# Optimization experiments

Hardware: AMD Instinct MI355X
Metric: run time of the kernel (lower is better)

## Reference

```python
import jax, jax.numpy as jnp
import numpy as np

WBITS_MAX = 3.0   # 3-bit signed narrow-range weights: levels in [-3, 3]
ABITS_MAX = 15.0  # 4-bit unsigned activations: levels in [0, 15]


def round_ste(x):
    # straight-through estimator for round (Brevitas uses STE)
    return x + jax.lax.stop_gradient(jnp.round(x) - x)


def quant_weight(w):
    # per-tensor symmetric narrow-range 3-bit fake quant (Int weight per-tensor float)
    s = jnp.max(jnp.abs(w)) / WBITS_MAX
    wq = jnp.clip(round_ste(w / s), -WBITS_MAX, WBITS_MAX) * s
    return wq, s


def quant_bias(b, w_scale, in_step):
    # Brevitas BiasQuant: bias scale = input_scale * weight_scale, no clipping (wide int)
    sb = w_scale * in_step  # in_step is shape (1,)
    return round_ste(b / sb) * sb


def quant_relu(x, s):
    # QuantReLU(bit_width=4): relu then unsigned 4-bit fake quant with learned scale s
    step = s / ABITS_MAX
    return jnp.clip(round_ste(jax.nn.relu(x) / step), 0.0, ABITS_MAX) * step


def conv2d(x, w):
    return jax.lax.conv_general_dilated(
        x, w, window_strides=(1, 1), padding='VALID',
        dimension_numbers=('NCHW', 'OIHW', 'NCHW'))


def maxpool2(x):
    return jax.lax.reduce_window(x, -jnp.inf, jax.lax.max,
                                 (1, 1, 2, 2), (1, 1, 2, 2), 'VALID')


def setup_inputs() -> dict:
    key = jax.random.key(0)
    ks = jax.random.split(key, 16)
    d = {}
    d['x'] = jax.random.normal(ks[0], (256, 3, 160, 160), jnp.float32)
    d['w1'] = jax.random.normal(ks[1], (6, 3, 3, 3), jnp.float32) * 0.2
    d['w2'] = jax.random.normal(ks[2], (12, 6, 3, 3), jnp.float32) * 0.2
    d['b2'] = jax.random.normal(ks[3], (12,), jnp.float32) * 0.1
    d['w3'] = jax.random.normal(ks[4], (18, 12, 3, 3), jnp.float32) * 0.2
    d['b3'] = jax.random.normal(ks[5], (18,), jnp.float32) * 0.1
    d['w4'] = jax.random.normal(ks[6], (18, 18, 3, 3), jnp.float32) * 0.2
    d['b4'] = jax.random.normal(ks[7], (18,), jnp.float32) * 0.1
    d['w5'] = jax.random.normal(ks[8], (18, 18, 3, 3), jnp.float32) * 0.2
    d['b5'] = jax.random.normal(ks[9], (18,), jnp.float32) * 0.1
    d['fw1'] = jax.random.normal(ks[10], (120, 162), jnp.float32) * 0.1
    d['fb1'] = jax.random.normal(ks[11], (120,), jnp.float32) * 0.1
    d['fw2'] = jax.random.normal(ks[12], (84, 120), jnp.float32) * 0.1
    d['fb2'] = jax.random.normal(ks[13], (84,), jnp.float32) * 0.1
    d['fw3'] = jax.random.normal(ks[14], (9, 84), jnp.float32) * 0.1
    for i in range(1, 8):
        d[f's{i}'] = jnp.full((1,), 6.0, jnp.float32)  # learned act scales (calibrated init)
    return d


def reference(x, w1, w2, b2, w3, b3, w4, b4, w5, b5,
              fw1, fb1, fw2, fb2, fw3, s1, s2, s3, s4, s5, s6, s7):
    # stage 1 (note: original forward feeds raw x into conv1, bypassing quant_inp)
    q1, _ = quant_weight(w1)
    out = maxpool2(quant_relu(conv2d(x, q1), s1))            # [B,6,79,79]
    # stage 2
    q2, ws2 = quant_weight(w2)
    bq2 = quant_bias(b2, ws2, s1 / ABITS_MAX)
    out = maxpool2(quant_relu(conv2d(out, q2) + bq2[None, :, None, None], s2))  # [B,12,38,38]
    # stage 3
    q3, ws3 = quant_weight(w3)
    bq3 = quant_bias(b3, ws3, s2 / ABITS_MAX)
    out = maxpool2(quant_relu(conv2d(out, q3) + bq3[None, :, None, None], s3))  # [B,18,18,18]
    # stage 4
    q4, ws4 = quant_weight(w4)
    bq4 = quant_bias(b4, ws4, s3 / ABITS_MAX)
    out = maxpool2(quant_relu(conv2d(out, q4) + bq4[None, :, None, None], s4))  # [B,18,8,8]
    # stage 5
    q5, ws5 = quant_weight(w5)
    bq5 = quant_bias(b5, ws5, s4 / ABITS_MAX)
    out = maxpool2(quant_relu(conv2d(out, q5) + bq5[None, :, None, None], s5))  # [B,18,3,3]
    out = out.reshape(out.shape[0], -1)                      # [B,162]
    # fc1
    qf1, fs1 = quant_weight(fw1)
    bqf1 = quant_bias(fb1, fs1, s5 / ABITS_MAX)
    out = quant_relu(out @ qf1.T + bqf1, s6)                 # [B,120]
    # fc2
    qf2, fs2 = quant_weight(fw2)
    bqf2 = quant_bias(fb2, fs2, s6 / ABITS_MAX)
    out = quant_relu(out @ qf2.T + bqf2, s7)                 # [B,84]
    # fc3 (no bias, output not re-quantized: return_quant_tensor=False default path)
    qf3, _ = quant_weight(fw3)
    return out @ qf3.T                                       # [B,9]
```

## Files before the change

### kernel.cpp

```cpp
#include <hip/hip_runtime.h>
#include <hip/hip_bf16.h>
#include <math.h>
#include <type_traits>

constexpr size_t OFF_OUT1B = 0;
constexpr size_t OFF_OUT2B = (size_t)256 * 6 * 79 * 80;
constexpr size_t OFF_A3B   = 0;

template<int CIN, int COUT, int NCO, int HIN, int WSIN,
         int HPOOL, int WPOOL, int WSOUT, int XG, int RB,
         int THREADS, bool HAS_BIAS, bool IN_U8>
__global__ __launch_bounds__(THREADS)
void conv_stage(const void* __restrict__ in_,
                const float* __restrict__ w_raw,
                const float* __restrict__ b_raw,
                const float* __restrict__ s_prev,
                const float* __restrict__ s_act,
                unsigned char* __restrict__ out)
{
    using TIN = typename std::conditional<IN_U8, unsigned char, float>::type;
    constexpr int GROUPS = COUT / NCO;
    constexpr int W4IN   = WSIN / 4;
    constexpr int NW     = COUT * CIN * 9;
    constexpr int STEPS  = 4 * CIN;
    static_assert(NCO * GROUPS == COUT, "NCO divides COUT");
    static_assert(GROUPS * XG * RB <= THREADS, "single compute pass");
    static_assert(4 * XG == WSOUT, "full padded row coverage");
    static_assert(WSIN % 4 == 0, "vec4 loads");

    __shared__ float lw[NW];
    __shared__ float lb[COUT];
    __shared__ float red[THREADS];

    const int r0  = blockIdx.x * RB;
    const int n   = blockIdx.y;
    const int tid = threadIdx.x;

    float mx = 0.0f;
    for (int i = tid; i < NW; i += THREADS) {
        const float v = w_raw[i];
        lw[i] = v;
        mx = fmaxf(mx, fabsf(v));
    }
    if (HAS_BIAS)
        for (int i = tid; i < COUT; i += THREADS) lb[i] = b_raw[i];
    red[tid] = mx;
    __syncthreads();
    for (int s = THREADS / 2; s > 0; s >>= 1) {
        if (tid < s) red[tid] = fmaxf(red[tid], red[tid + s]);
        __syncthreads();
    }
    const float sw_ = red[0] / 3.0f;
    for (int i = tid; i < NW; i += THREADS) {
        float q = rintf(lw[i] / sw_);
        q = fminf(fmaxf(q, -3.0f), 3.0f);
        lw[i] = q * sw_;
    }
    if (HAS_BIAS) {
        const float sb = sw_ * (s_prev[0] / 15.0f);
        for (int i = tid; i < COUT; i += THREADS)
            lb[i] = rintf(lb[i] / sb) * sb;
    }
    __syncthreads();

    const int o = tid;
    if (o >= GROUPS * XG * RB) return;
    const int cog = o % GROUPS;
    const int xg  = (o / GROUPS) % XG;
    const int ry  = o / (GROUPS * XG);
    const int r   = r0 + ry;
    if (r >= HPOOL) return;

    const float step = s_act[0] / 15.0f;
    float step_in = 0.0f;
    if constexpr (IN_U8) step_in = s_prev[0] / 15.0f;

    const int u0 = 2 * xg;
    const int u1 = 2 * xg + 1;
    const int u2 = (2 * xg + 2 < W4IN) ? (2 * xg + 2) : (W4IN - 1);

    const TIN* in   = (const TIN*)in_;
    const TIN* base = in + (size_t)n * CIN * HIN * WSIN + (size_t)(2 * r) * WSIN;

    float acc[NCO][16];
#pragma unroll
    for (int j = 0; j < NCO; ++j)
#pragma unroll
        for (int i = 0; i < 16; ++i) acc[j][i] = 0.0f;

    float4       fbuf[3][3];
    unsigned int ubuf[3][3];
    float        wv[NCO][9];

#define ISSUE_STEP(S)                                                          \
    {                                                                          \
        const TIN* rp = base + (size_t)((S) >> 2) * HIN * WSIN                 \
                             + (size_t)((S) & 3) * WSIN;                       \
        if constexpr (IN_U8) {                                                 \
            ubuf[(S) % 3][0] = *(const unsigned int*)&rp[4 * u0];              \
            ubuf[(S) % 3][1] = *(const unsigned int*)&rp[4 * u1];              \
            ubuf[(S) % 3][2] = *(const unsigned int*)&rp[4 * u2];              \
        } else {                                                               \
            fbuf[(S) % 3][0] = *(const float4*)&rp[4 * u0];                    \
            fbuf[(S) % 3][1] = *(const float4*)&rp[4 * u1];                    \
            fbuf[(S) % 3][2] = *(const float4*)&rp[4 * u2];                    \
        }                                                                      \
    }

    ISSUE_STEP(0);
    ISSUE_STEP(1);

#pragma unroll
    for (int s = 0; s < STEPS; ++s) {
        const int c  = s >> 2;
        const int rr = s & 3;

        if (s + 2 < STEPS) ISSUE_STEP(s + 2);

        if (rr == 0) {
#pragma unroll
            for (int j = 0; j < NCO; ++j)
#pragma unroll
                for (int k = 0; k < 9; ++k)
                    wv[j][k] = lw[((NCO * cog + j) * CIN + c) * 9 + k];
        }

        float row[12];
        if constexpr (IN_U8) {
#pragma unroll
            for (int k = 0; k < 3; ++k) {
                const unsigned int d = ubuf[s % 3][k];
#pragma unroll
                for (int b = 0; b < 4; ++b)
                    row[4 * k + b] = (float)((d >> (8 * b)) & 0xffu) * step_in;
            }
        } else {
            const float* rv = (const float*)fbuf[s % 3];
#pragma unroll
            for (int i = 0; i < 12; ++i) row[i] = rv[i];
        }

        if (rr < 3) {
#pragma unroll
            for (int j = 0; j < NCO; ++j)
#pragma unroll
                for (int kc = 0; kc < 3; ++kc)
#pragma unroll
                    for (int xx = 0; xx < 8; ++xx)
                        acc[j][xx] = fmaf(row[xx + kc], wv[j][rr * 3 + kc], acc[j][xx]);
        }
        if (rr >= 1) {
#pragma unroll
            for (int j = 0; j < NCO; ++j)
#pragma unroll
                for (int kc = 0; kc < 3; ++kc)
#pragma unroll
                    for (int xx = 0; xx < 8; ++xx)
                        acc[j][8 + xx] = fmaf(row[xx + kc], wv[j][(rr - 1) * 3 + kc], acc[j][8 + xx]);
        }
    }
#undef ISSUE_STEP

#pragma unroll
    for (int j = 0; j < NCO; ++j) {
        const int co = NCO * cog + j;
        const float bias = HAS_BIAS ? lb[co] : 0.0f;
        unsigned int pck = 0;
#pragma unroll
        for (int t = 0; t < 4; ++t) {
            float m = fmaxf(fmaxf(acc[j][2 * t], acc[j][2 * t + 1]),
                            fmaxf(acc[j][8 + 2 * t], acc[j][8 + 2 * t + 1]));
            float v = fmaxf(m + bias, 0.0f);
            float q = rintf(v / step);
            q = fminf(fmaxf(q, 0.0f), 15.0f);
            const unsigned int qi = (4 * xg + t < WPOOL) ? (unsigned int)q : 0u;
            pck |= qi << (8 * t);
        }
        *(unsigned int*)&out[(((size_t)n * COUT + co) * HPOOL + r) * WSOUT + 4 * xg] = pck;
    }
}

__device__ __forceinline__ float wave_max(float v) {
#pragma unroll
    for (int off = 32; off > 0; off >>= 1)
        v = fmaxf(v, __shfl_down(v, off));
    return v;
}

__global__ __launch_bounds__(512)
void conv3_stage(const unsigned char* __restrict__ in2,
                 const float* __restrict__ w3, const float* __restrict__ b3,
                 const float* __restrict__ s2, const float* __restrict__ s3,
                 float* __restrict__ a3)
{
    __shared__ float lw[1944];
    __shared__ float lb[18];
    __shared__ float red[512];

    const int rb  = blockIdx.x;
    const int n   = blockIdx.y;
    const int tid = threadIdx.x;

    float mx = 0.0f;
    for (int i = tid; i < 1944; i += 512) {
        const float v = w3[i];
        lw[i] = v;
        mx = fmaxf(mx, fabsf(v));
    }
    if (tid < 18) lb[tid] = b3[tid];
    red[tid] = mx;
    __syncthreads();
    for (int s = 256; s > 0; s >>= 1) {
        if (tid < s) red[tid] = fmaxf(red[tid], red[tid + s]);
        __syncthreads();
    }
    const float sw = red[0] / 3.0f;
    for (int i = tid; i < 1944; i += 512) {
        float q = rintf(lw[i] / sw);
        q = fminf(fmaxf(q, -3.0f), 3.0f);
        lw[i] = q * sw;
    }
    if (tid < 18) {
        const float sb = sw * (s2[0] / 15.0f);
        lb[tid] = rintf(lb[tid] / sb) * sb;
    }
    __syncthreads();

    if (tid >= 486) return;
    const int rloc = tid / 54;
    const int rm   = tid - rloc * 54;
    const int co   = rm / 3;
    const int th   = rm - co * 3;
    const int r    = rb * 9 + rloc;

    const float step2 = s2[0] / 15.0f;
    const float st    = s3[0] / 15.0f;

    const unsigned char* base = in2 + (size_t)n * 18240 + (size_t)(2 * r) * 40 + 12 * th;

    float acc0[12], acc1[12];
#pragma unroll
    for (int i = 0; i < 12; ++i) { acc0[i] = 0.f; acc1[i] = 0.f; }

    unsigned int ub[2][16];

#define LOADC(C, B)                                                            \
    {                                                                          \
        const unsigned char* cp = base + (size_t)(C) * 1520;                   \
        _Pragma("unroll")                                                      \
        for (int rr = 0; rr < 4; ++rr)                                         \
            _Pragma("unroll")                                                  \
            for (int k = 0; k < 4; ++k)                                        \
                ub[B][rr * 4 + k] = *(const unsigned int*)&cp[rr * 40 + 4 * k];\
    }

    LOADC(0, 0);

#pragma unroll
    for (int c = 0; c < 12; ++c) {
        if (c + 1 < 12) LOADC(c + 1, (c + 1) & 1);

        float wv[9];
#pragma unroll
        for (int k = 0; k < 9; ++k) wv[k] = lw[(co * 12 + c) * 9 + k];

#pragma unroll
        for (int rr = 0; rr < 4; ++rr) {
            float row[16];
#pragma unroll
            for (int k = 0; k < 4; ++k) {
                const unsigned int d = ub[c & 1][rr * 4 + k];
#pragma unroll
                for (int b = 0; b < 4; ++b)
                    row[4 * k + b] = (float)((d >> (8 * b)) & 0xffu) * step2;
            }
            if (rr < 3) {
#pragma unroll
                for (int kc = 0; kc < 3; ++kc)
#pragma unroll
                    for (int xx = 0; xx < 12; ++xx)
                        acc0[xx] = fmaf(row[xx + kc], wv[rr * 3 + kc], acc0[xx]);
            }
            if (rr >= 1) {
#pragma unroll
                for (int kc = 0; kc < 3; ++kc)
#pragma unroll
                    for (int xx = 0; xx < 12; ++xx)
                        acc1[xx] = fmaf(row[xx + kc], wv[(rr - 1) * 3 + kc], acc1[xx]);
            }
        }
    }
#undef LOADC

    const float bias = lb[co];
    float* orow = a3 + (size_t)n * 5832 + (size_t)co * 324 + (size_t)r * 18 + 6 * th;
#pragma unroll
    for (int x = 0; x < 6; ++x) {
        float m = fmaxf(fmaxf(acc0[2 * x], acc0[2 * x + 1]),
                        fmaxf(acc1[2 * x], acc1[2 * x + 1]));
        float v = fmaxf(m + bias, 0.0f);
        float q = rintf(v / st);
        q = fminf(fmaxf(q, 0.0f), 15.0f);
        orow[x] = q * st;
    }
}

__global__ __launch_bounds__(1024)
void tail456(const float* __restrict__ a3in,
             const float* __restrict__ w4, const float* __restrict__ b4,
             const float* __restrict__ w5, const float* __restrict__ b5,
             const float* __restrict__ fw1, const float* __restrict__ fb1,
             const float* __restrict__ fw2, const float* __restrict__ fb2,
             const float* __restrict__ fw3,
             const float* __restrict__ s3, const float* __restrict__ s4,
             const float* __restrict__ s5, const float* __restrict__ s6,
             const float* __restrict__ s7,
             float* __restrict__ out)
{
    __shared__ float A3[5832];
    __shared__ float W4q[2916], W5q[2916];
    __shared__ float B4q[18], B5q[18];
    __shared__ float O4t[64 * 19 + 1];
    __shared__ float A5[162], A6[120], A7[84];
    __shared__ float part[8][120];
    __shared__ float sm[16][5];
    __shared__ float scales[5];

    const int n    = blockIdx.x;
    const int tid  = threadIdx.x;
    const int wid  = tid >> 6;
    const int lane = tid & 63;

    {
        const float4* src = (const float4*)(a3in + (size_t)n * 5832);
        float4* dst = (float4*)A3;
        for (int i = tid; i < 1458; i += 1024) dst[i] = src[i];
    }
    float m4 = 0.f, m5 = 0.f, g1 = 0.f, g2 = 0.f, g3 = 0.f;
    for (int i = tid; i < 2916; i += 1024) { const float v = w4[i]; W4q[i] = v; m4 = fmaxf(m4, fabsf(v)); }
    for (int i = tid; i < 2916; i += 1024) { const float v = w5[i]; W5q[i] = v; m5 = fmaxf(m5, fabsf(v)); }
    {
        const float4* f1 = (const float4*)fw1;
        for (int i = tid; i < 4860; i += 1024) {
            const float4 v = f1[i];
            g1 = fmaxf(g1, fmaxf(fmaxf(fabsf(v.x), fabsf(v.y)), fmaxf(fabsf(v.z), fabsf(v.w))));
        }
        const float4* f2 = (const float4*)fw2;
        for (int i = tid; i < 2520; i += 1024) {
            const float4 v = f2[i];
            g2 = fmaxf(g2, fmaxf(fmaxf(fabsf(v.x), fabsf(v.y)), fmaxf(fabsf(v.z), fabsf(v.w))));
        }
        const float4* f3 = (const float4*)fw3;
        for (int i = tid; i < 189; i += 1024) {
            const float4 v = f3[i];
            g3 = fmaxf(g3, fmaxf(fmaxf(fabsf(v.x), fabsf(v.y)), fmaxf(fabsf(v.z), fabsf(v.w))));
        }
    }
    if (tid < 18) { B4q[tid] = b4[tid]; B5q[tid] = b5[tid]; }
    m4 = wave_max(m4); m5 = wave_max(m5);
    g1 = wave_max(g1); g2 = wave_max(g2); g3 = wave_max(g3);
    if (lane == 0) {
        sm[wid][0] = m4; sm[wid][1] = m5;
        sm[wid][2] = g1; sm[wid][3] = g2; sm[wid][4] = g3;
    }
    __syncthreads();
    if (tid < 5) {
        float v = sm[0][tid];
#pragma unroll
        for (int w = 1; w < 16; ++w) v = fmaxf(v, sm[w][tid]);
        scales[tid] = v / 3.0f;
    }
    __syncthreads();
    const float sw4 = scales[0], sw5 = scales[1];
    const float sf1 = scales[2], sf2 = scales[3], sf3 = scales[4];

    for (int i = tid; i < 2916; i += 1024) { float q = rintf(W4q[i] / sw4); q = fminf(fmaxf(q, -3.f), 3.f); W4q[i] = q * sw4; }
    for (int i = tid; i < 2916; i += 1024) { float q = rintf(W5q[i] / sw5); q = fminf(fmaxf(q, -3.f), 3.f); W5q[i] = q * sw5; }
    if (tid < 18) {
        const float sb4 = sw4 * (s3[0] / 15.0f); B4q[tid] = rintf(B4q[tid] / sb4) * sb4;
        const float sb5 = sw5 * (s4[0] / 15.0f); B5q[tid] = rintf(B5q[tid] / sb5) * sb5;
    }
    __syncthreads();

    {
        const float st = s4[0] / 15.0f;
        for (int o = tid; o < 1152; o += 1024) {
            const int co = o >> 6;
            const int r  = (o >> 3) & 7;
            const int x  = o & 7;
            float a00 = 0.f, a01 = 0.f, a10 = 0.f, a11 = 0.f;
            for (int c = 0; c < 18; ++c) {
                float win[4][4];
#pragma unroll
                for (int rr = 0; rr < 4; ++rr) {
                    const int base = c * 324 + (2 * r + rr) * 18 + 2 * x;
                    *(float2*)&win[rr][0] = *(const float2*)&A3[base];
                    *(float2*)&win[rr][2] = *(const float2*)&A3[base + 2];
                }
                const float* wp = &W4q[(co * 18 + c) * 9];
#pragma unroll
                for (int kr = 0; kr < 3; ++kr)
#pragma unroll
                    for (int kc = 0; kc < 3; ++kc) {
                        const float wvv = wp[kr * 3 + kc];
                        a00 = fmaf(win[kr    ][kc    ], wvv, a00);
                        a01 = fmaf(win[kr    ][kc + 1], wvv, a01);
                        a10 = fmaf(win[kr + 1][kc    ], wvv, a10);
                        a11 = fmaf(win[kr + 1][kc + 1], wvv, a11);
                    }
            }
            float m = fmaxf(fmaxf(a00, a01), fmaxf(a10, a11));
            float v = fmaxf(m + B4q[co], 0.0f);
            float q = rintf(v / st);
            q = fminf(fmaxf(q, 0.0f), 15.0f);
            O4t[(r * 8 + x) * 19 + co] = q * st;
        }
    }
    __syncthreads();

    {
        const float st = s5[0] / 15.0f;
        if (tid < 162) {
            const int co  = tid / 9;
            const int rem = tid - co * 9;
            const int r   = rem / 3;
            const int x   = rem - r * 3;
            float a00 = 0.f, a01 = 0.f, a10 = 0.f, a11 = 0.f;
            for (int c = 0; c < 18; ++c) {
                float win[4][4];
#pragma unroll
                for (int rr = 0; rr < 4; ++rr)
#pragma unroll
                    for (int cc = 0; cc < 4; ++cc)
                        win[rr][cc] = O4t[((2 * r + rr) * 8 + 2 * x + cc) * 19 + c];
                const float* wp = &W5q[(co * 18 + c) * 9];
#pragma unroll
                for (int kr = 0; kr < 3; ++kr)
#pragma unroll
                    for (int kc = 0; kc < 3; ++kc) {
                        const float wvv = wp[kr * 3 + kc];
                        a00 = fmaf(win[kr    ][kc    ], wvv, a00);
                        a01 = fmaf(win[kr    ][kc + 1], wvv, a01);
                        a10 = fmaf(win[kr + 1][kc    ], wvv, a10);
                        a11 = fmaf(win[kr + 1][kc + 1], wvv, a11);
                    }
            }
            float m = fmaxf(fmaxf(a00, a01), fmaxf(a10, a11));
            float v = fmaxf(m + B5q[co], 0.0f);
            float q = rintf(v / st);
            q = fminf(fmaxf(q, 0.0f), 15.0f);
            A5[tid] = q * st;
        }
    }
    __syncthreads();

    if (tid < 960) {
        const int m  = tid % 120;
        const int ch = tid / 120;
        const int k0 = 21 * ch;
        const int k1 = (ch == 7) ? 162 : k0 + 21;
        float p = 0.f;
        const float* wr = fw1 + (size_t)m * 162;
        for (int k = k0; k < k1; ++k) {
            float q = rintf(wr[k] / sf1);
            q = fminf(fmaxf(q, -3.f), 3.f);
            p = fmaf(A5[k], q * sf1, p);
        }
        part[ch][m] = p;
    }
    __syncthreads();
    if (tid < 120) {
        float acc = part[0][tid];
#pragma unroll
        for (int ch = 1; ch < 8; ++ch) acc += part[ch][tid];
        const float sb = sf1 * (s5[0] / 15.0f);
        acc += rintf(fb1[tid] / sb) * sb;
        const float st = s6[0] / 15.0f;
        float q = rintf(fmaxf(acc, 0.0f) / st);
        q = fminf(fmaxf(q, 0.0f), 15.0f);
        A6[tid] = q * st;
    }
    __syncthreads();

    if (tid < 672) {
        const int m  = tid % 84;
        const int ch = tid / 84;
        const int k0 = 15 * ch;
        float p = 0.f;
        const float* wr = fw2 + (size_t)m * 120;
        for (int k = k0; k < k0 + 15; ++k) {
            float q = rintf(wr[k] / sf2);
            q = fminf(fmaxf(q, -3.f), 3.f);
            p = fmaf(A6[k], q * sf2, p);
        }
        part[ch][m] = p;
    }
    __syncthreads();
    if (tid < 84) {
        float acc = part[0][tid];
#pragma unroll
        for (int ch = 1; ch < 8; ++ch) acc += part[ch][tid];
        const float sb = sf2 * (s6[0] / 15.0f);
        acc += rintf(fb2[tid] / sb) * sb;
        const float st = s7[0] / 15.0f;
        float q = rintf(fmaxf(acc, 0.0f) / st);
        q = fminf(fmaxf(q, 0.0f), 15.0f);
        A7[tid] = q * st;
    }
    __syncthreads();

    if (tid < 63) {
        const int m  = tid % 9;
        const int ch = tid / 9;
        const int k0 = 12 * ch;
        float p = 0.f;
        const float* wr = fw3 + (size_t)m * 84;
        for (int k = k0; k < k0 + 12; ++k) {
            float q = rintf(wr[k] / sf3);
            q = fminf(fmaxf(q, -3.f), 3.f);
            p = fmaf(A7[k], q * sf3, p);
        }
        part[ch][m] = p;
    }
    __syncthreads();
    if (tid < 9) {
        float acc = part[0][tid];
#pragma unroll
        for (int ch = 1; ch < 7; ++ch) acc += part[ch][tid];
        out[(size_t)n * 9 + tid] = acc;
    }
}

extern "C" void kernel_launch(void* const* d_in, const int* in_sizes, int n_in,
                              void* d_out, int out_size, void* d_ws, size_t ws_size,
                              hipStream_t stream)
{
    const float* x   = (const float*)d_in[0];
    const float* w1  = (const float*)d_in[1];
    const float* w2  = (const float*)d_in[2];
    const float* b2  = (const float*)d_in[3];
    const float* w3  = (const float*)d_in[4];
    const float* b3  = (const float*)d_in[5];
    const float* w4  = (const float*)d_in[6];
    const float* b4  = (const float*)d_in[7];
    const float* w5  = (const float*)d_in[8];
    const float* b5  = (const float*)d_in[9];
    const float* fw1 = (const float*)d_in[10];
    const float* fb1 = (const float*)d_in[11];
    const float* fw2 = (const float*)d_in[12];
    const float* fb2 = (const float*)d_in[13];
    const float* fw3 = (const float*)d_in[14];
    const float* s1  = (const float*)d_in[15];
    const float* s2  = (const float*)d_in[16];
    const float* s3  = (const float*)d_in[17];
    const float* s4  = (const float*)d_in[18];
    const float* s5  = (const float*)d_in[19];
    const float* s6  = (const float*)d_in[20];
    const float* s7  = (const float*)d_in[21];

    unsigned char* wsb = (unsigned char*)d_ws;
    float* out = (float*)d_out;

    conv_stage<3, 6, 2, 160, 160, 79, 79, 80, 20, 4, 256, false, false>
        <<<dim3(20, 256), 256, 0, stream>>>(x, w1, nullptr, nullptr, s1,
                                            wsb + OFF_OUT1B);

    conv_stage<6, 12, 2, 79, 80, 38, 38, 40, 10, 4, 256, true, true>
        <<<dim3(10, 256), 256, 0, stream>>>(wsb + OFF_OUT1B, w2, b2, s1, s2,
                                            wsb + OFF_OUT2B);

    conv3_stage<<<dim3(2, 256), 512, 0, stream>>>(wsb + OFF_OUT2B, w3, b3, s2, s3,
                                                  (float*)(wsb + OFF_A3B));

    tail456<<<256, 1024, 0, stream>>>((const float*)(wsb + OFF_A3B),
                                      w4, b4, w5, b5,
                                      fw1, fb1, fw2, fb2, fw3,
                                      s3, s4, s5, s6, s7, out);
}
```

Before: 141.4 us.

## Hoist weight quantization into a prep kernel and store conv3 output as uint8

Adds a small prep kernel that fake-quantizes all conv3-5 and FC weights and biases once per call, with FC weights transposed for coalesced access. This replaces the per-block max-abs reductions and requantization that conv3 and tail456 repeated in all 512 and 256 blocks. Conv3 now writes 4-bit activation levels as bytes instead of floats, cutting that intermediate's traffic by four, and tail456 dequantizes them into a padded shared layout. The cost is one extra kernel launch and a serial dependency on prep.

Result: slower. 150.8 us (+6.7%).

```diff
diff --git a/kernel.cpp b/kernel.cpp
--- a/kernel.cpp
+++ b/kernel.cpp
@@ -6,6 +6,106 @@
 constexpr size_t OFF_OUT1B = 0;
 constexpr size_t OFF_OUT2B = (size_t)256 * 6 * 79 * 80;
 constexpr size_t OFF_A3B   = 0;
+constexpr size_t OFF_WQ    = OFF_OUT2B + (size_t)256 * 12 * 38 * 40;
+
+constexpr int QW3  = 0;
+constexpr int QB3  = 1944;
+constexpr int QW4  = 1968;
+constexpr int QB4  = 4884;
+constexpr int QW5  = 4904;
+constexpr int QB5  = 7820;
+constexpr int QF1  = 7840;
+constexpr int QFB1 = 27280;
+constexpr int QF2  = 27400;
+constexpr int QFB2 = 37480;
+constexpr int QF3  = 37568;
+
+__device__ float block_max_abs(const float* p, int n, int tid, float* red) {
+    float m = 0.0f;
+    for (int i = tid; i < n; i += 256) m = fmaxf(m, fabsf(p[i]));
+    red[tid] = m;
+    __syncthreads();
+    for (int s = 128; s > 0; s >>= 1) {
+        if (tid < s) red[tid] = fmaxf(red[tid], red[tid + s]);
+        __syncthreads();
+    }
+    const float r = red[0];
+    __syncthreads();
+    return r;
+}
+
+__global__ __launch_bounds__(256)
+void prep(const float* __restrict__ w3, const float* __restrict__ b3,
+          const float* __restrict__ w4, const float* __restrict__ b4,
+          const float* __restrict__ w5, const float* __restrict__ b5,
+          const float* __restrict__ fw1, const float* __restrict__ fb1,
+          const float* __restrict__ fw2, const float* __restrict__ fb2,
+          const float* __restrict__ fw3,
+          const float* __restrict__ s2, const float* __restrict__ s3,
+          const float* __restrict__ s4, const float* __restrict__ s5,
+          const float* __restrict__ s6,
+          float* __restrict__ wq)
+{
+    __shared__ float red[256];
+    const int b   = blockIdx.x;
+    const int tid = threadIdx.x;
+
+    if (b == 0) {
+        const float s = block_max_abs(w3, 1944, tid, red) / 3.0f;
+        for (int i = tid; i < 1944; i += 256) {
+            float q = rintf(w3[i] / s); q = fminf(fmaxf(q, -3.f), 3.f);
+            wq[QW3 + i] = q * s;
+        }
+    } else if (b == 1) {
+        const float s = block_max_abs(w4, 2916, tid, red) / 3.0f;
+        for (int i = tid; i < 2916; i += 256) {
+            float q = rintf(w4[i] / s); q = fminf(fmaxf(q, -3.f), 3.f);
+            wq[QW4 + i] = q * s;
+        }
+    } else if (b == 2) {
+        const float s = block_max_abs(w5, 2916, tid, red) / 3.0f;
+        for (int i = tid; i < 2916; i += 256) {
+            float q = rintf(w5[i] / s); q = fminf(fmaxf(q, -3.f), 3.f);
+            wq[QW5 + i] = q * s;
+        }
+    } else if (b <= 10) {
+        const float s = block_max_abs(fw1, 19440, tid, red) / 3.0f;
+        const int sl = b - 3;
+        const int lo = 19440 * sl / 8, hi = 19440 * (sl + 1) / 8;
+        for (int i = lo + tid; i < hi; i += 256) {
+            const int m = i / 162, k = i - m * 162;
+            float q = rintf(fw1[i] / s); q = fminf(fmaxf(q, -3.f), 3.f);
+            wq[QF1 + k * 120 + m] = q * s;
+        }
+    } else if (b <= 14) {
+        const float s = block_max_abs(fw2, 10080, tid, red) / 3.0f;
+        const int sl = b - 11;
+        const int lo = 10080 * sl / 4, hi = 10080 * (sl + 1) / 4;
+        for (int i = lo + tid; i < hi; i += 256) {
+            const int m = i / 120, k = i - m * 120;
+            float q = rintf(fw2[i] / s); q = fminf(fmaxf(q, -3.f), 3.f);
+            wq[QF2 + k * 84 + m] = q * s;
+        }
+    } else if (b == 15) {
+        const float s = block_max_abs(fw3, 756, tid, red) / 3.0f;
+        for (int i = tid; i < 756; i += 256) {
+            const int m = i / 84, k = i - m * 84;
+            float q = rintf(fw3[i] / s); q = fminf(fmaxf(q, -3.f), 3.f);
+            wq[QF3 + k * 9 + m] = q * s;
+        }
+    } else {
+        const float s3w = block_max_abs(w3, 1944, tid, red) / 3.0f;
+        const float s4w = block_max_abs(w4, 2916, tid, red) / 3.0f;
+        const float s5w = block_max_abs(w5, 2916, tid, red) / 3.0f;
+        const float sg1 = block_max_abs(fw1, 19440, tid, red) / 3.0f;
+        const float sg2 = block_max_abs(fw2, 10080, tid, red) / 3.0f;
+        if (tid < 18)  { const float sb = s3w * (s2[0] / 15.f); wq[QB3 + tid]  = rintf(b3[tid] / sb) * sb; }
+        if (tid < 18)  { const float sb = s4w * (s3[0] / 15.f); wq[QB4 + tid]  = rintf(b4[tid] / sb) * sb; }
+        if (tid < 18)  { const float sb = s5w * (s4[0] / 15.f); wq[QB5 + tid]  = rintf(b5[tid] / sb) * sb; }
+        if (tid < 120) { const float sb = sg1 * (s5[0] / 15.f); wq[QFB1 + tid] = rintf(fb1[tid] / sb) * sb; }
+        if (tid < 84)  { const float sb = sg2 * (s6[0] / 15.f); wq[QFB2 + tid] = rintf(fb2[tid] / sb) * sb; }
+    }
+}
 
 template<int CIN, int COUT, int NCO, int HIN, int WSIN,
          int HPOOL, int WPOOL, int WSOUT, int XG, int RB,
@@ -180,50 +280,21 @@
     }
 }
 
-__device__ __forceinline__ float wave_max(float v) {
-#pragma unroll
-    for (int off = 32; off > 0; off >>= 1)
-        v = fmaxf(v, __shfl_down(v, off));
-    return v;
-}
-
 __global__ __launch_bounds__(512)
 void conv3_stage(const unsigned char* __restrict__ in2,
-                 const float* __restrict__ w3, const float* __restrict__ b3,
+                 const float* __restrict__ wq,
                  const float* __restrict__ s2, const float* __restrict__ s3,
-                 float* __restrict__ a3)
+                 unsigned char* __restrict__ a3u)
 {
     __shared__ float lw[1944];
     __shared__ float lb[18];
-    __shared__ float red[512];
 
     const int rb  = blockIdx.x;
     const int n   = blockIdx.y;
     const int tid = threadIdx.x;
 
-    float mx = 0.0f;
-    for (int i = tid; i < 1944; i += 512) {
-        const float v = w3[i];
-        lw[i] = v;
-        mx = fmaxf(mx, fabsf(v));
-    }
-    if (tid < 18) lb[tid] = b3[tid];
-    red[tid] = mx;
-    __syncthreads();
-    for (int s = 256; s > 0; s >>= 1) {
-        if (tid < s) red[tid] = fmaxf(red[tid], red[tid + s]);
-        __syncthreads();
-    }
-    const float sw = red[0] / 3.0f;
-    for (int i = tid; i < 1944; i += 512) {
-        float q = rintf(lw[i] / sw);
-        q = fminf(fmaxf(q, -3.0f), 3.0f);
-        lw[i] = q * sw;
-    }
-    if (tid < 18) {
-        const float sb = sw * (s2[0] / 15.0f);
-        lb[tid] = rintf(lb[tid] / sb) * sb;
-    }
+    for (int i = tid; i < 1944; i += 512) lw[i] = wq[QW3 + i];
+    if (tid < 18) lb[tid] = wq[QB3 + tid];
     __syncthreads();
 
     if (tid >= 486) return;
@@ -242,16 +313,14 @@
 #pragma unroll
     for (int i = 0; i < 12; ++i) { acc0[i] = 0.f; acc1[i] = 0.f; }
 
-    unsigned int ub[2][16];
+    uint4 ub[2][4];
 
 #define LOADC(C, B)                                                            \
     {                                                                          \
         const unsigned char* cp = base + (size_t)(C) * 1520;                   \
         _Pragma("unroll")                                                      \
         for (int rr = 0; rr < 4; ++rr)                                         \
-            _Pragma("unroll")                                                  \
-            for (int k = 0; k < 4; ++k)                                        \
-                ub[B][rr * 4 + k] = *(const unsigned int*)&cp[rr * 40 + 4 * k];\
+            __builtin_memcpy(&ub[B][rr], cp + rr * 40, 16);                    \
     }
 
     LOADC(0, 0);
@@ -266,10 +335,11 @@
 
 #pragma unroll
         for (int rr = 0; rr < 4; ++rr) {
+            const unsigned int* dp = (const unsigned int*)&ub[c & 1][rr];
             float row[16];
 #pragma unroll
             for (int k = 0; k < 4; ++k) {
-                const unsigned int d = ub[c & 1][rr * 4 + k];
+                const unsigned int d = dp[k];
 #pragma unroll
                 for (int b = 0; b < 4; ++b)
                     row[4 * k + b] = (float)((d >> (8 * b)) & 0xffu) * step2;
@@ -293,7 +363,7 @@
 #undef LOADC
 
     const float bias = lb[co];
-    float* orow = a3 + (size_t)n * 5832 + (size_t)co * 324 + (size_t)r * 18 + 6 * th;
+    unsigned char* orow = a3u + (size_t)n * 5832 + (size_t)co * 324 + (size_t)r * 18 + 6 * th;
 #pragma unroll
     for (int x = 0; x < 6; ++x) {
         float m = fmaxf(fmaxf(acc0[2 * x], acc0[2 * x + 1]),
@@ -301,85 +371,47 @@
         float v = fmaxf(m + bias, 0.0f);
         float q = rintf(v / st);
         q = fminf(fmaxf(q, 0.0f), 15.0f);
-        orow[x] = q * st;
+        orow[x] = (unsigned char)q;
     }
 }
 
 __global__ __launch_bounds__(1024)
-void tail456(const float* __restrict__ a3in,
-             const float* __restrict__ w4, const float* __restrict__ b4,
-             const float* __restrict__ w5, const float* __restrict__ b5,
-             const float* __restrict__ fw1, const float* __restrict__ fb1,
-             const float* __restrict__ fw2, const float* __restrict__ fb2,
-             const float* __restrict__ fw3,
+void tail456(const unsigned char* __restrict__ a3u,
+             const float* __restrict__ wq,
              const float* __restrict__ s3, const float* __restrict__ s4,
              const float* __restrict__ s5, const float* __restrict__ s6,
              const float* __restrict__ s7,
              float* __restrict__ out)
 {
-    __shared__ float A3[5832];
+    __shared__ float A3f[18 * 18 * 20];
     __shared__ float W4q[2916], W5q[2916];
     __shared__ float B4q[18], B5q[18];
     __shared__ float O4t[64 * 19 + 1];
     __shared__ float A5[162], A6[120], A7[84];
     __shared__ float part[8][120];
-    __shared__ float sm[16][5];
-    __shared__ float scales[5];
-
-    const int n    = blockIdx.x;
-    const int tid  = threadIdx.x;
-    const int wid  = tid >> 6;
-    const int lane = tid & 63;
-
+
+    const int n   = blockIdx.x;
+    const int tid = threadIdx.x;
+
+    const float st3 = s3[0] / 15.0f;
     {
-        const float4* src = (const float4*)(a3in + (size_t)n * 5832);
-        float4* dst = (float4*)A3;
-        for (int i = tid; i < 1458; i += 1024) dst[i] = src[i];
-    }
-    float m4 = 0.f, m5 = 0.f, g1 = 0.f, g2 = 0.f, g3 = 0.f;
-    for (int i = tid; i < 2916; i += 1024) { const float v = w4[i]; W4q[i] = v; m4 = fmaxf(m4, fabsf(v)); }
-    for (int i = tid; i < 2916; i += 1024) { const float v = w5[i]; W5q[i] = v; m5 = fmaxf(m5, fabsf(v)); }
-    {
-        const float4* f1 = (const float4*)fw1;
-        for (int i = tid; i < 4860; i += 1024) {
-            const float4 v = f1[i];
-            g1 = fmaxf(g1, fmaxf(fmaxf(fabsf(v.x), fabsf(v.y)), fmaxf(fabsf(v.z), fabsf(v.w))));
-        }
-        const float4* f2 = (const float4*)fw2;
-        for (int i = tid; i < 2520; i += 1024) {
-            const float4 v = f2[i];
-            g2 = fmaxf(g2, fmaxf(fmaxf(fabsf(v.x), fabsf(v.y)), fmaxf(fabsf(v.z), fabsf(v.w))));
-        }
-        const float4* f3 = (const float4*)fw3;
-        for (int i = tid; i < 189; i += 1024) {
-            const float4 v = f3[i];
-            g3 = fmaxf(g3, fmaxf(fmaxf(fabsf(v.x), fabsf(v.y)), fmaxf(fabsf(v.z), fabsf(v.w))));
-        }
-    }
-    if (tid < 18) { B4q[tid] = b4[tid]; B5q[tid] = b5[tid]; }
-    m4 = wave_max(m4); m5 = wave_max(m5);
-    g1 = wave_max(g1); g2 = wave_max(g2); g3 = wave_max(g3);
-    if (lane == 0) {
-        sm[wid][0] = m4; sm[wid][1] = m5;
-        sm[wid][2] = g1; sm[wid][3] = g2; sm[wid][4] = g3;
-    }
-    __syncthreads();
-    if (tid < 5) {
-        float v = sm[0][tid];
-#pragma unroll
-        for (int w = 1; w < 16; ++w) v = fmaxf(v, sm[w][tid]);
-        scales[tid] = v / 3.0f;
-    }
-    __syncthreads();
-    const float sw4 = scales[0], sw5 = scales[1];
-    const float sf1 = scales[2], sf2 = scales[3], sf3 = scales[4];
-
-    for (int i = tid; i < 2916; i += 1024) { float q = rintf(W4q[i] / sw4); q = fminf(fmaxf(q, -3.f), 3.f); W4q[i] = q * sw4; }
-    for (int i = tid; i < 2916; i += 1024) { float q = rintf(W5q[i] / sw5); q = fminf(fmaxf(q, -3.f), 3.f); W5q[i] = q * sw5; }
-    if (tid < 18) {
-        const float sb4 = sw4 * (s3[0] / 15.0f); B4q[tid] = rintf(B4q[tid] / sb4) * sb4;
-        const float sb5 = sw5 * (s4[0] / 15.0f); B5q[tid] = rintf(B5q[tid] / sb5) * sb5;
-    }
+        const unsigned int* src = (const unsigned int*)(a3u + (size_t)n * 5832);
+        for (int i = tid; i < 1458; i += 1024) {
+            const unsigned int d = src[i];
+#pragma unroll
+            for (int b = 0; b < 4; ++b) {
+                const int idx = 4 * i + b;
+                const int co  = idx / 324;
+                const int rem = idx - co * 324;
+                const int r   = rem / 18;
+                const int x   = rem - r * 18;
+                A3f[(co * 18 + r) * 20 + x] = (float)((d >> (8 * b)) & 0xffu) * st3;
+            }
+        }
+    }
+    for (int i = tid; i < 2916; i += 1024) W4q[i] = wq[QW4 + i];
+    for (int i = tid; i < 2916; i += 1024) W5q[i] = wq[QW5 + i];
+    if (tid < 18) { B4q[tid] = wq[QB4 + tid]; B5q[tid] = wq[QB5 + tid]; }
     __syncthreads();
 
     {
@@ -393,9 +425,9 @@
                 float win[4][4];
 #pragma unroll
                 for (int rr = 0; rr < 4; ++rr) {
-                    const int base = c * 324 + (2 * r + rr) * 18 + 2 * x;
-                    *(float2*)&win[rr][0] = *(const float2*)&A3[base];
-                    *(float2*)&win[rr][2] = *(const float2*)&A3[base + 2];
+                    const int base = (c * 18 + 2 * r + rr) * 20 + 2 * x;
+                    *(float2*)&win[rr][0] = *(const float2*)&A3f[base];
+                    *(float2*)&win[rr][2] = *(const float2*)&A3f[base + 2];
                 }
                 const float* wp = &W4q[(co * 18 + c) * 9];
 #pragma unroll
@@ -454,27 +486,25 @@
     }
     __syncthreads();
 
-    if (tid < 960) {
-        const int m  = tid % 120;
-        const int ch = tid / 120;
-        const int k0 = 21 * ch;
-        const int k1 = (ch == 7) ? 162 : k0 + 21;
-        float p = 0.f;
-        const float* wr = fw1 + (size_t)m * 162;
-        for (int k = k0; k < k1; ++k) {
-            float q = rintf(wr[k] / sf1);
-            q = fminf(fmaxf(q, -3.f), 3.f);
-            p = fmaf(A5[k], q * sf1, p);
-        }
-        part[ch][m] = p;
+    {
+        const float* F1 = wq + QF1;
+        if (tid < 960) {
+            const int m  = tid % 120;
+            const int ch = tid / 120;
+            const int k0 = 21 * ch;
+            const int k1 = (ch == 7) ? 162 : k0 + 21;
+            float p = 0.f;
+            for (int k = k0; k < k1; ++k)
+                p = fmaf(A5[k], F1[k * 120 + m], p);
+            part[ch][m] = p;
+        }
     }
     __syncthreads();
     if (tid < 120) {
         float acc = part[0][tid];
 #pragma unroll
         for (int ch = 1; ch < 8; ++ch) acc += part[ch][tid];
-        const float sb = sf1 * (s5[0] / 15.0f);
-        acc += rintf(fb1[tid] / sb) * sb;
+        acc += wq[QFB1 + tid];
         const float st = s6[0] / 15.0f;
         float q = rintf(fmaxf(acc, 0.0f) / st);
         q = fminf(fmaxf(q, 0.0f), 15.0f);
@@ -482,26 +512,24 @@
     }
     __syncthreads();
 
-    if (tid < 672) {
-        const int m  = tid % 84;
-        const int ch = tid / 84;
-        const int k0 = 15 * ch;
-        float p = 0.f;
-        const float* wr = fw2 + (size_t)m * 120;
-        for (int k = k0; k < k0 + 15; ++k) {
-            float q = rintf(wr[k] / sf2);
-            q = fminf(fmaxf(q, -3.f), 3.f);
-            p = fmaf(A6[k], q * sf2, p);
-        }
-        part[ch][m] = p;
+    {
+        const float* F2 = wq + QF2;
+        if (tid < 672) {
+            const int m  = tid % 84;
+            const int ch = tid / 84;
+            const int k0 = 15 * ch;
+            float p = 0.f;
+            for (int k = k0; k < k0 + 15; ++k)
+                p = fmaf(A6[k], F2[k * 84 + m], p);
+            part[ch][m] = p;
+        }
     }
     __syncthreads();
     if (tid < 84) {
         float acc = part[0][tid];
 #pragma unroll
         for (int ch = 1; ch < 8; ++ch) acc += part[ch][tid];
-        const float sb = sf2 * (s6[0] / 15.0f);
-        acc += rintf(fb2[tid] / sb) * sb;
+        acc += wq[QFB2 + tid];
         const float st = s7[0] / 15.0f;
         float q = rintf(fmaxf(acc, 0.0f) / st);
         q = fminf(fmaxf(q, 0.0f), 15.0f);
@@ -509,18 +537,17 @@
     }
     __syncthreads();
 
-    if (tid < 63) {
-        const int m  = tid % 9;
-        const int ch = tid / 9;
-        const int k0 = 12 * ch;
-        float p = 0.f;
-        const float* wr = fw3 + (size_t)m * 84;
-        for (int k = k0; k < k0 + 12; ++k) {
-            float q = rintf(wr[k] / sf3);
-            q = fminf(fmaxf(q, -3.f), 3.f);
-            p = fmaf(A7[k], q * sf3, p);
-        }
-        part[ch][m] = p;
+    {
+        const float* F3 = wq + QF3;
+        if (tid < 63) {
+            const int m  = tid % 9;
+            const int ch = tid / 9;
+            const int k0 = 12 * ch;
+            float p = 0.f;
+            for (int k = k0; k < k0 + 12; ++k)
+                p = fmaf(A7[k], F3[k * 9 + m], p);
+            part[ch][m] = p;
+        }
     }
     __syncthreads();
     if (tid < 9) {
@@ -559,7 +586,12 @@
     const float* s7  = (const float*)d_in[21];
 
     unsigned char* wsb = (unsigned char*)d_ws;
+    float* wq = (float*)(wsb + OFF_WQ);
     float* out = (float*)d_out;
+
+    prep<<<17, 256, 0, stream>>>(w3, b3, w4, b4, w5, b5,
+                                 fw1, fb1, fw2, fb2, fw3,
+                                 s2, s3, s4, s5, s6, wq);
 
     conv_stage<3, 6, 2, 160, 160, 79, 79, 80, 20, 4, 256, false, false>
         <<<dim3(20, 256), 256, 0, stream>>>(x, w1, nullptr, nullptr, s1,
@@ -569,11 +601,9 @@
         <<<dim3(10, 256), 256, 0, stream>>>(wsb + OFF_OUT1B, w2, b2, s1, s2,
                                             wsb + OFF_OUT2B);
 
-    conv3_stage<<<dim3(2, 256), 512, 0, stream>>>(wsb + OFF_OUT2B, w3, b3, s2, s3,
-                                                  (float*)(wsb + OFF_A3B));
-
-    tail456<<<256, 1024, 0, stream>>>((const float*)(wsb + OFF_A3B),
-                                      w4, b4, w5, b5,
-                                      fw1, fb1, fw2, fb2, fw3,
+    conv3_stage<<<dim3(2, 256), 512, 0, stream>>>(wsb + OFF_OUT2B, wq, s2, s3,
+                                                  wsb + OFF_A3B);
+
+    tail456<<<256, 1024, 0, stream>>>(wsb + OFF_A3B, wq,
                                       s3, s4, s5, s6, s7, out);
 }
```
